# Performance work log

Measured on AMD Instinct MI355X. Metric: run time of the kernel, lower is better.

## Reference

```python
import jax, jax.numpy as jnp
import numpy as np
from jax.scipy.special import logsumexp

K, V, D, R = 512, 50257, 768, 192
S_ITERS = 10
LAMBDA_MAHAL = 0.3
GAMMA_SINKHORN = 0.3


def setup_inputs() -> dict:
    key = jax.random.key(0)
    ks = jax.random.split(key, 6)
    word_embeds = jax.random.normal(ks[0], (V, D), dtype=jnp.float32)
    # warm-start anchors: mean word embed + small noise (as in torch init)
    anchors = jnp.broadcast_to(word_embeds.mean(axis=0, keepdims=True), (K, D)) \
        + jax.random.normal(ks[1], (K, D), dtype=jnp.float32) * 0.05
    return {
        "word_embeds": word_embeds,
        "concept_anchors": anchors,
        "M_U": jax.random.normal(ks[2], (D, R), dtype=jnp.float32) * 0.01,
        "log_eps": jnp.float32(-1.5),
        "log_scale": jnp.float32(0.0),
        "topic_bias": jnp.zeros((K, 1), dtype=jnp.float32),
        "word_proj_w": jnp.eye(D, dtype=jnp.float32),
    }


def _normalize(x, eps=1e-12):
    n = jnp.sqrt(jnp.sum(x * x, axis=-1, keepdims=True))
    return x / jnp.maximum(n, eps)


def _mahalanobis_cost(A, B, M_U):
    # M = I + U U^T  (low-rank update); C[k,v] = (a-b)^T M (a-b)
    M = jnp.eye(A.shape[-1], dtype=A.dtype) + M_U @ M_U.T
    MA = A @ M          # [K, D]
    MB = B @ M          # [V, D]
    AA = jnp.sum(MA * A, axis=-1, keepdims=True)       # [K, 1]
    BB = jnp.sum(MB * B, axis=-1, keepdims=True).T     # [1, V]
    AB = MA @ B.T                                      # [K, V]
    return jax.nn.relu(AA + BB - 2.0 * AB)


def _sinkhorn_log(log_K):
    def body(_, carry):
        log_u, log_v = carry
        log_u = -logsumexp(log_K + log_v, axis=1, keepdims=True)  # [K,1]
        log_v = -logsumexp(log_K + log_u, axis=0, keepdims=True)  # [1,V]
        return log_u, log_v
    log_u0 = jnp.zeros((log_K.shape[0], 1), log_K.dtype)
    log_v0 = jnp.zeros((1, log_K.shape[1]), log_K.dtype)
    log_u, log_v = jax.lax.fori_loop(0, S_ITERS, body, (log_u0, log_v0))
    return log_K + log_u + log_v


def reference(word_embeds, concept_anchors, M_U, log_eps, log_scale,
              topic_bias, word_proj_w):
    w = _normalize(word_embeds @ word_proj_w.T)     # [V, D]
    a = _normalize(concept_anchors)                 # [K, D]
    scale = jnp.minimum(jnp.exp(log_scale), 20.0)
    direct_logits = scale * (a @ w.T) + topic_bias  # [K, V]
    mahal = _mahalanobis_cost(a, w, M_U)            # [K, V]
    eps = jax.nn.softplus(log_eps) + 0.001
    log_P = _sinkhorn_log(-mahal / eps)             # [K, V]
    logits = direct_logits - LAMBDA_MAHAL * mahal + GAMMA_SINKHORN * log_P
    logits = jnp.clip(logits, -30.0, 30.0)
    return jax.nn.softmax(logits, axis=-1)
```

## Files before the change

kernel.cpp:

```cpp
#include <hip/hip_runtime.h>
#include <math.h>

#define KK 512
#define VV 50257
#define VP 50272
#define DD 768
#define RR 192

#define LAM 0.3f
#define GAM 0.3f
#define L2E 1.44269504088896340736f
#define ENC_NEG_INF 0x007FFFFFu

typedef __bf16 bf16x8 __attribute__((ext_vector_type(8)));
typedef _Float16 f16x8 __attribute__((ext_vector_type(8)));
typedef _Float16 f16x2 __attribute__((ext_vector_type(2)));
typedef unsigned short u16x8 __attribute__((ext_vector_type(8)));
typedef float f32x4 __attribute__((ext_vector_type(4)));

static __device__ __forceinline__ float get_eps(const float* p_log_eps) {
  return log1pf(expf(p_log_eps[0])) + 0.001f;
}

static __device__ __forceinline__ float fast_exp2(float x) {
  return __builtin_amdgcn_exp2f(x);
}

static __device__ __forceinline__ unsigned enc_f(float f) {
  unsigned u = __builtin_bit_cast(unsigned, f);
  return (u & 0x80000000u) ? ~u : (u | 0x80000000u);
}
static __device__ __forceinline__ float dec_f(unsigned e) {
  unsigned u = (e & 0x80000000u) ? (e ^ 0x80000000u) : ~e;
  return __builtin_bit_cast(float, u);
}

static __device__ __forceinline__ unsigned short f2bf(float x) {
  unsigned u = __builtin_bit_cast(unsigned, x);
  u += 0x7fffu + ((u >> 16) & 1u);
  return (unsigned short)(u >> 16);
}
static __device__ __forceinline__ float bf2f(unsigned short h) {
  unsigned u = ((unsigned)h) << 16;
  return __builtin_bit_cast(float, u);
}

__global__ __launch_bounds__(256)
void prep(const float* __restrict__ U, float* __restrict__ lv2,
          unsigned* __restrict__ slots, const float* __restrict__ anchors,
          _Float16* __restrict__ Ut16, _Float16* __restrict__ a16) {
  int bid = blockIdx.x;
  int t = threadIdx.x;
  if (bid < 576) {
    int idx = bid * 256 + t;
    int r = idx / DD;
    int d = idx - r * DD;
    Ut16[idx] = (_Float16)U[(size_t)d * RR + r];
  } else if (bid < 773) {
    int i = (bid - 576) * 256 + t;
    if (i < 50264) lv2[i] = 0.f;
  } else if (bid == 773) {
    if (t < 24) slots[t] = (t == 0) ? 0x80000000u : ENC_NEG_INF;
    if (t == 24) slots[24] = 1u;
  } else {
    int r = bid - 774;
    const float* x = anchors + (size_t)r * DD;
    float v0 = x[t], v1 = x[t + 256], v2 = x[t + 512];
    __shared__ float red[256];
    red[t] = v0 * v0 + v1 * v1 + v2 * v2;
    __syncthreads();
    for (int off = 128; off > 0; off >>= 1) {
      if (t < off) red[t] += red[t + off];
      __syncthreads();
    }
    float inv = 1.0f / fmaxf(sqrtf(red[0]), 1e-12f);
    _Float16* y = a16 + (size_t)r * DD;
    y[t] = (_Float16)(v0 * inv);
    y[t + 256] = (_Float16)(v1 * inv);
    y[t + 512] = (_Float16)(v2 * inv);
  }
}

__global__ __launch_bounds__(256)
void check_eye(const float* __restrict__ Wp, unsigned* __restrict__ flag) {
  int i = blockIdx.x * 256 + threadIdx.x;
  if (i >= DD * DD) return;
  int r = i / DD;
  int c = i - r * DD;
  float expect = (r == c) ? 1.f : 0.f;
  if (Wp[i] != expect) atomicAnd(flag, 0u);
}

#define BM 128
#define BN 128
#define BK 32
#define LDKB 40
#define LDK 40

__global__ __launch_bounds__(256, 2)
void gemm_we_fallback(const float* __restrict__ A, const float* __restrict__ B,
                      _Float16* __restrict__ C, int M, int N, int Kd,
                      const unsigned* __restrict__ eyeflag) {
  if (*eyeflag) return;
  __shared__ unsigned short As[2][BM][LDKB];
  __shared__ unsigned short Bs[2][BN][LDKB];
  const int tid = threadIdx.x;
  const int bm = blockIdx.y * BM;
  const int bn = blockIdx.x * BN;
  const int srow = tid >> 1;
  const int skb = (tid & 1) << 4;
  const int wave = tid >> 6;
  const int lane = tid & 63;
  const int wm = (wave >> 1) << 6;
  const int wn = (wave & 1) << 6;
  const int lm = lane & 15;
  const int quad = lane >> 4;
  f32x4 acc[4][4];
#pragma unroll
  for (int i = 0; i < 4; ++i)
#pragma unroll
    for (int j = 0; j < 4; ++j) acc[i][j] = (f32x4){0.f, 0.f, 0.f, 0.f};
  const int ra = bm + srow;
  const int rb = bn + srow;
  for (int k0 = 0; k0 < Kd; k0 += BK) {
    float va[16], vb[16];
    if (ra < M) {
      const float4* p = (const float4*)(A + (size_t)ra * Kd + k0 + skb);
      ((float4*)va)[0] = p[0]; ((float4*)va)[1] = p[1];
      ((float4*)va)[2] = p[2]; ((float4*)va)[3] = p[3];
    } else {
#pragma unroll
      for (int q = 0; q < 16; ++q) va[q] = 0.f;
    }
    if (rb < N) {
      const float4* p = (const float4*)(B + (size_t)rb * Kd + k0 + skb);
      ((float4*)vb)[0] = p[0]; ((float4*)vb)[1] = p[1];
      ((float4*)vb)[2] = p[2]; ((float4*)vb)[3] = p[3];
    } else {
#pragma unroll
      for (int q = 0; q < 16; ++q) vb[q] = 0.f;
    }
    __syncthreads();
    {
      u16x8 h0, h1, l0, l1;
#pragma unroll
      for (int q = 0; q < 8; ++q) {
        unsigned short h = f2bf(va[q]);
        h0[q] = h; l0[q] = f2bf(va[q] - bf2f(h));
        h = f2bf(va[q + 8]);
        h1[q] = h; l1[q] = f2bf(va[q + 8] - bf2f(h));
      }
      *(u16x8*)&As[0][srow][skb] = h0; *(u16x8*)&As[0][srow][skb + 8] = h1;
      *(u16x8*)&As[1][srow][skb] = l0; *(u16x8*)&As[1][srow][skb + 8] = l1;
#pragma unroll
      for (int q = 0; q < 8; ++q) {
        unsigned short h = f2bf(vb[q]);
        h0[q] = h; l0[q] = f2bf(vb[q] - bf2f(h));
        h = f2bf(vb[q + 8]);
        h1[q] = h; l1[q] = f2bf(vb[q + 8] - bf2f(h));
      }
      *(u16x8*)&Bs[0][srow][skb] = h0; *(u16x8*)&Bs[0][srow][skb + 8] = h1;
      *(u16x8*)&Bs[1][srow][skb] = l0; *(u16x8*)&Bs[1][srow][skb + 8] = l1;
    }
    __syncthreads();
    bf16x8 Ah[4], Al[4], Bh[4], Bl[4];
#pragma unroll
    for (int i = 0; i < 4; ++i) {
      Ah[i] = *(const bf16x8*)&As[0][wm + i * 16 + lm][quad * 8];
      Al[i] = *(const bf16x8*)&As[1][wm + i * 16 + lm][quad * 8];
      Bh[i] = *(const bf16x8*)&Bs[0][wn + i * 16 + lm][quad * 8];
      Bl[i] = *(const bf16x8*)&Bs[1][wn + i * 16 + lm][quad * 8];
    }
#pragma unroll
    for (int i = 0; i < 4; ++i)
#pragma unroll
      for (int j = 0; j < 4; ++j) {
        acc[i][j] = __builtin_amdgcn_mfma_f32_16x16x32_bf16(Ah[i], Bh[j], acc[i][j], 0, 0, 0);
        acc[i][j] = __builtin_amdgcn_mfma_f32_16x16x32_bf16(Ah[i], Bl[j], acc[i][j], 0, 0, 0);
        acc[i][j] = __builtin_amdgcn_mfma_f32_16x16x32_bf16(Al[i], Bh[j], acc[i][j], 0, 0, 0);
      }
  }
#pragma unroll
  for (int i = 0; i < 4; ++i)
#pragma unroll
    for (int j = 0; j < 4; ++j) {
      int col = bn + wn + j * 16 + lm;
#pragma unroll
      for (int r = 0; r < 4; ++r) {
        int row = bm + wm + i * 16 + quad * 4 + r;
        if (row < M && col < N) C[(size_t)row * N + col] = (_Float16)acc[i][j][r];
      }
    }
}

__global__ __launch_bounds__(256)
void norm_w(const float* __restrict__ WE, _Float16* __restrict__ w16,
            const unsigned* __restrict__ eyeflag) {
  int r = blockIdx.x;
  int t = threadIdx.x;
  float v0, v1, v2;
  if (*eyeflag) {
    const float* x = WE + (size_t)r * DD;
    v0 = x[t]; v1 = x[t + 256]; v2 = x[t + 512];
  } else {
    const _Float16* x = w16 + (size_t)r * DD;
    v0 = (float)x[t]; v1 = (float)x[t + 256]; v2 = (float)x[t + 512];
  }
  __shared__ float red[256];
  red[t] = v0 * v0 + v1 * v1 + v2 * v2;
  __syncthreads();
  for (int off = 128; off > 0; off >>= 1) {
    if (t < off) red[t] += red[t + off];
    __syncthreads();
  }
  float inv = 1.0f / fmaxf(sqrtf(red[0]), 1e-12f);
  _Float16* y = w16 + (size_t)r * DD;
  y[t] = (_Float16)(v0 * inv);
  y[t + 256] = (_Float16)(v1 * inv);
  y[t + 512] = (_Float16)(v2 * inv);
}

template <int F16OUT>
__global__ __launch_bounds__(256, 2)
void gemm16(const _Float16* __restrict__ A, const _Float16* __restrict__ B,
            void* __restrict__ Cv, int M, int N, int Kd) {
  __shared__ _Float16 As[BM][LDK];
  __shared__ _Float16 Bs[BN][LDK];
  const int tid = threadIdx.x;
  const int bm = blockIdx.y * BM;
  const int bn = blockIdx.x * BN;
  const int srow = tid >> 1;
  const int skb = (tid & 1) << 4;
  const int wave = tid >> 6;
  const int lane = tid & 63;
  const int wm = (wave >> 1) << 6;
  const int wn = (wave & 1) << 6;
  const int lm = lane & 15;
  const int quad = lane >> 4;
  f32x4 acc[4][4];
#pragma unroll
  for (int i = 0; i < 4; ++i)
#pragma unroll
    for (int j = 0; j < 4; ++j) acc[i][j] = (f32x4){0.f, 0.f, 0.f, 0.f};
  const int ra = bm + srow;
  const int rb = bn + srow;
  for (int k0 = 0; k0 < Kd; k0 += BK) {
    f16x8 a0 = (f16x8)(_Float16)0, a1 = a0, b0 = a0, b1 = a0;
    if (ra < M) {
      const f16x8* p = (const f16x8*)(A + (size_t)ra * Kd + k0 + skb);
      a0 = p[0]; a1 = p[1];
    }
    if (rb < N) {
      const f16x8* p = (const f16x8*)(B + (size_t)rb * Kd + k0 + skb);
      b0 = p[0]; b1 = p[1];
    }
    __syncthreads();
    *(f16x8*)&As[srow][skb] = a0; *(f16x8*)&As[srow][skb + 8] = a1;
    *(f16x8*)&Bs[srow][skb] = b0; *(f16x8*)&Bs[srow][skb + 8] = b1;
    __syncthreads();
    f16x8 Af[4], Bf[4];
#pragma unroll
    for (int i = 0; i < 4; ++i) {
      Af[i] = *(const f16x8*)&As[wm + i * 16 + lm][quad * 8];
      Bf[i] = *(const f16x8*)&Bs[wn + i * 16 + lm][quad * 8];
    }
#pragma unroll
    for (int i = 0; i < 4; ++i)
#pragma unroll
      for (int j = 0; j < 4; ++j)
        acc[i][j] = __builtin_amdgcn_mfma_f32_16x16x32_f16(Af[i], Bf[j], acc[i][j], 0, 0, 0);
  }
#pragma unroll
  for (int i = 0; i < 4; ++i)
#pragma unroll
    for (int j = 0; j < 4; ++j) {
      int col = bn + wn + j * 16 + lm;
#pragma unroll
      for (int r = 0; r < 4; ++r) {
        int row = bm + wm + i * 16 + quad * 4 + r;
        if (row < M && col < N) {
          if (F16OUT)
            ((_Float16*)Cv)[(size_t)row * N + col] = (_Float16)acc[i][j][r];
          else
            ((float*)Cv)[(size_t)row * N + col] = acc[i][j][r];
        }
      }
    }
}

__global__ __launch_bounds__(256, 2)
void gemm_sp(const _Float16* __restrict__ Aw, const _Float16* __restrict__ Bw,
             const _Float16* __restrict__ Au, const _Float16* __restrict__ Bu,
             float* __restrict__ Sd, _Float16* __restrict__ mhq,
             const float* __restrict__ AAv, const float* __restrict__ BBv,
             const float* __restrict__ tbias,
             const float* __restrict__ p_log_scale,
             const float* __restrict__ p_log_eps, int M, int N) {
  __shared__ _Float16 As[BM][LDK];
  __shared__ _Float16 Bs[BN][LDK];
  const int tid = threadIdx.x;
  const int bm = blockIdx.y * BM;
  const int bn = blockIdx.x * BN;
  const int srow = tid >> 1;
  const int skb = (tid & 1) << 4;
  const int wave = tid >> 6;
  const int lane = tid & 63;
  const int wm = (wave >> 1) << 6;
  const int wn = (wave & 1) << 6;
  const int lm = lane & 15;
  const int quad = lane >> 4;
  const int ra = bm + srow;
  const int rb = bn + srow;
  f32x4 accP[4][4];
#pragma unroll
  for (int i = 0; i < 4; ++i)
#pragma unroll
    for (int j = 0; j < 4; ++j) accP[i][j] = (f32x4){0.f, 0.f, 0.f, 0.f};
  for (int k0 = 0; k0 < RR; k0 += BK) {
    f16x8 a0 = (f16x8)(_Float16)0, a1 = a0, b0 = a0, b1 = a0;
    if (ra < M) {
      const f16x8* p = (const f16x8*)(Au + (size_t)ra * RR + k0 + skb);
      a0 = p[0]; a1 = p[1];
    }
    if (rb < N) {
      const f16x8* p = (const f16x8*)(Bu + (size_t)rb * RR + k0 + skb);
      b0 = p[0]; b1 = p[1];
    }
    __syncthreads();
    *(f16x8*)&As[srow][skb] = a0; *(f16x8*)&As[srow][skb + 8] = a1;
    *(f16x8*)&Bs[srow][skb] = b0; *(f16x8*)&Bs[srow][skb + 8] = b1;
    __syncthreads();
    f16x8 Af[4], Bf[4];
#pragma unroll
    for (int i = 0; i < 4; ++i) {
      Af[i] = *(const f16x8*)&As[wm + i * 16 + lm][quad * 8];
      Bf[i] = *(const f16x8*)&Bs[wn + i * 16 + lm][quad * 8];
    }
#pragma unroll
    for (int i = 0; i < 4; ++i)
#pragma unroll
      for (int j = 0; j < 4; ++j)
        accP[i][j] = __builtin_amdgcn_mfma_f32_16x16x32_f16(Af[i], Bf[j], accP[i][j], 0, 0, 0);
  }
  f32x4 accS[4][4];
#pragma unroll
  for (int i = 0; i < 4; ++i)
#pragma unroll
    for (int j = 0; j < 4; ++j) accS[i][j] = (f32x4){0.f, 0.f, 0.f, 0.f};
  for (int k0 = 0; k0 < DD; k0 += BK) {
    f16x8 a0 = (f16x8)(_Float16)0, a1 = a0, b0 = a0, b1 = a0;
    if (ra < M) {
      const f16x8* p = (const f16x8*)(Aw + (size_t)ra * DD + k0 + skb);
      a0 = p[0]; a1 = p[1];
    }
    if (rb < N) {
      const f16x8* p = (const f16x8*)(Bw + (size_t)rb * DD + k0 + skb);
      b0 = p[0]; b1 = p[1];
    }
    __syncthreads();
    *(f16x8*)&As[srow][skb] = a0; *(f16x8*)&As[srow][skb + 8] = a1;
    *(f16x8*)&Bs[srow][skb] = b0; *(f16x8*)&Bs[srow][skb + 8] = b1;
    __syncthreads();
    f16x8 Af[4], Bf[4];
#pragma unroll
    for (int i = 0; i < 4; ++i) {
      Af[i] = *(const f16x8*)&As[wm + i * 16 + lm][quad * 8];
      Bf[i] = *(const f16x8*)&Bs[wn + i * 16 + lm][quad * 8];
    }
#pragma unroll
    for (int i = 0; i < 4; ++i)
#pragma unroll
      for (int j = 0; j < 4; ++j)
        accS[i][j] = __builtin_amdgcn_mfma_f32_16x16x32_f16(Af[i], Bf[j], accS[i][j], 0, 0, 0);
  }
  float scale = fminf(expf(p_log_scale[0]), 20.f);
  float qs = L2E / get_eps(p_log_eps);
#pragma unroll
  for (int i = 0; i < 4; ++i)
#pragma unroll
    for (int j = 0; j < 4; ++j) {
      int col = bn + wn + j * 16 + lm;
      if (col >= N) continue;
      float BB = BBv[col];
#pragma unroll
      for (int r = 0; r < 4; ++r) {
        int row = bm + wm + i * 16 + quad * 4 + r;
        float S = accS[i][j][r];
        float mh = fmaxf(AAv[row] + BB - 2.f * (S + accP[i][j][r]), 0.f);
        Sd[(size_t)row * N + col] = fmaf(scale, S, tbias[row]);
        mhq[(size_t)row * VP + col] = (_Float16)(mh * qs);
      }
    }
}

__global__ __launch_bounds__(256, 2)
void gemm16_p(const _Float16* __restrict__ A, const _Float16* __restrict__ B,
              float* __restrict__ Sd, _Float16* __restrict__ mhq,
              const float* __restrict__ AAv, const float* __restrict__ BBv,
              const float* __restrict__ tbias,
              const float* __restrict__ p_log_scale,
              const float* __restrict__ p_log_eps, int M, int N, int Kd) {
  __shared__ _Float16 As[BM][LDK];
  __shared__ _Float16 Bs[BN][LDK];
  const int tid = threadIdx.x;
  const int bm = blockIdx.y * BM;
  const int bn = blockIdx.x * BN;
  const int srow = tid >> 1;
  const int skb = (tid & 1) << 4;
  const int wave = tid >> 6;
  const int lane = tid & 63;
  const int wm = (wave >> 1) << 6;
  const int wn = (wave & 1) << 6;
  const int lm = lane & 15;
  const int quad = lane >> 4;
  f32x4 acc[4][4];
#pragma unroll
  for (int i = 0; i < 4; ++i)
#pragma unroll
    for (int j = 0; j < 4; ++j) acc[i][j] = (f32x4){0.f, 0.f, 0.f, 0.f};
  const int ra = bm + srow;
  const int rb = bn + srow;
  for (int k0 = 0; k0 < Kd; k0 += BK) {
    f16x8 a0 = (f16x8)(_Float16)0, a1 = a0, b0 = a0, b1 = a0;
    if (ra < M) {
      const f16x8* p = (const f16x8*)(A + (size_t)ra * Kd + k0 + skb);
      a0 = p[0]; a1 = p[1];
    }
    if (rb < N) {
      const f16x8* p = (const f16x8*)(B + (size_t)rb * Kd + k0 + skb);
      b0 = p[0]; b1 = p[1];
    }
    __syncthreads();
    *(f16x8*)&As[srow][skb] = a0; *(f16x8*)&As[srow][skb + 8] = a1;
    *(f16x8*)&Bs[srow][skb] = b0; *(f16x8*)&Bs[srow][skb + 8] = b1;
    __syncthreads();
    f16x8 Af[4], Bf[4];
#pragma unroll
    for (int i = 0; i < 4; ++i) {
      Af[i] = *(const f16x8*)&As[wm + i * 16 + lm][quad * 8];
      Bf[i] = *(const f16x8*)&Bs[wn + i * 16 + lm][quad * 8];
    }
#pragma unroll
    for (int i = 0; i < 4; ++i)
#pragma unroll
      for (int j = 0; j < 4; ++j)
        acc[i][j] = __builtin_amdgcn_mfma_f32_16x16x32_f16(Af[i], Bf[j], acc[i][j], 0, 0, 0);
  }
  float scale = fminf(expf(p_log_scale[0]), 20.f);
  float qs = L2E / get_eps(p_log_eps);
#pragma unroll
  for (int i = 0; i < 4; ++i)
#pragma unroll
    for (int j = 0; j < 4; ++j) {
      int col = bn + wn + j * 16 + lm;
      if (col >= N) continue;
      float BB = BBv[col];
#pragma unroll
      for (int r = 0; r < 4; ++r) {
        int row = bm + wm + i * 16 + quad * 4 + r;
        size_t idx = (size_t)row * N + col;
        float S = Sd[idx];
        float mh = fmaxf(AAv[row] + BB - 2.f * (S + acc[i][j][r]), 0.f);
        Sd[idx] = fmaf(scale, S, tbias[row]);
        mhq[(size_t)row * VP + col] = (_Float16)(mh * qs);
      }
    }
}

__global__ __launch_bounds__(256)
void row_sumsq16(const _Float16* __restrict__ X, float* __restrict__ out, int cols) {
  int r = blockIdx.x;
  int t = threadIdx.x;
  float x = (t < cols) ? (float)X[(size_t)r * cols + t] : 0.f;
  __shared__ float red[256];
  red[t] = x * x;
  __syncthreads();
  for (int off = 128; off > 0; off >>= 1) {
    if (t < off) red[t] += red[t + off];
    __syncthreads();
  }
  if (t == 0) out[r] = 1.0f + red[0];
}

__global__ __launch_bounds__(1024)
void sink_row(const _Float16* __restrict__ mhq, const float* __restrict__ lv2,
              float* __restrict__ lu2,
              const unsigned* __restrict__ Mv_slot, unsigned* __restrict__ Mu_slot) {
  int k = blockIdx.x;
  int t = threadIdx.x;
  float Mv2 = dec_f(*Mv_slot);
  const _Float16* row = mhq + (size_t)k * VP;
  float s[8] = {0.f, 0.f, 0.f, 0.f, 0.f, 0.f, 0.f, 0.f};
#pragma unroll
  for (int j = 0; j < 6; ++j) {
    int v = j * 8192 + t * 8;
    f16x8 hv = *(const f16x8*)(row + v);
    float4 l0 = *(const float4*)(lv2 + v);
    float4 l1 = *(const float4*)(lv2 + v + 4);
    float lv[8] = {l0.x, l0.y, l0.z, l0.w, l1.x, l1.y, l1.z, l1.w};
#pragma unroll
    for (int i = 0; i < 8; ++i)
      s[i] += fast_exp2(lv[i] - Mv2 - (float)hv[i]);
  }
  {
    int v = 49152 + t;
    s[0] += fast_exp2(lv2[v] - Mv2 - (float)row[v]);
    v = 50176 + t;
    if (v < VV) s[1] += fast_exp2(lv2[v] - Mv2 - (float)row[v]);
  }
  float sum = ((s[0] + s[1]) + (s[2] + s[3])) + ((s[4] + s[5]) + (s[6] + s[7]));
  __shared__ float red[1024];
  red[t] = sum;
  __syncthreads();
  for (int off = 512; off > 0; off >>= 1) {
    if (t < off) red[t] += red[t + off];
    __syncthreads();
  }
  if (t == 0) {
    float lu = -(Mv2 + log2f(red[0]));
    lu2[k] = lu;
    atomicMax(Mu_slot, enc_f(lu));
  }
}

__global__ __launch_bounds__(256)
void sink_col(const _Float16* __restrict__ mhq, const float* __restrict__ lu2,
              float* __restrict__ lv2,
              const unsigned* __restrict__ Mu_slot, unsigned* __restrict__ Mv_next) {
  __shared__ float lu_s[KK];
  int t = threadIdx.x;
  for (int i = t; i < KK; i += 256) lu_s[i] = lu2[i];
  __syncthreads();
  float Mu2 = dec_f(*Mu_slot);
  int cp = blockIdx.x * 64 + (t & 63);
  int v0 = cp * 2;
  int kc = t >> 6;
  float sA = 0.f, sB = 0.f;
  if (v0 < VV) {
    const _Float16* base = mhq + v0;
#pragma unroll 4
    for (int k = kc * 128; k < kc * 128 + 128; ++k) {
      f16x2 hv = *(const f16x2*)(base + (size_t)k * VP);
      float lu = lu_s[k] - Mu2;
      sA += fast_exp2(lu - (float)hv[0]);
      sB += fast_exp2(lu - (float)hv[1]);
    }
  }
  __shared__ float pA[256], pB[256];
  __shared__ unsigned em[64];
  pA[t] = sA; pB[t] = sB;
  __syncthreads();
  if (t < 64) {
    unsigned e = ENC_NEG_INF;
    if (v0 < VV) {
      float a = (pA[t] + pA[t + 64]) + (pA[t + 128] + pA[t + 192]);
      float lv = -(Mu2 + log2f(a));
      lv2[v0] = lv;
      e = enc_f(lv);
      if (v0 + 1 < VV) {
        float b = (pB[t] + pB[t + 64]) + (pB[t + 128] + pB[t + 192]);
        float lv1 = -(Mu2 + log2f(b));
        lv2[v0 + 1] = lv1;
        unsigned e1 = enc_f(lv1);
        if (e1 > e) e = e1;
      }
    }
    em[t] = e;
  }
  __syncthreads();
  for (int off = 32; off > 0; off >>= 1) {
    if (t < off && em[t + off] > em[t]) em[t] = em[t + off];
    __syncthreads();
  }
  if (t == 0) atomicMax(Mv_next, em[0]);
}

__global__ __launch_bounds__(1024)
void final_sum(const float* __restrict__ direct, const _Float16* __restrict__ mhq,
               const float* __restrict__ lu2, const float* __restrict__ lv2,
               float* __restrict__ row_s, const float* __restrict__ p_log_eps) {
  int k = blockIdx.x;
  int t = threadIdx.x;
  float eps = get_eps(p_log_eps);
  float c2 = (LAM * eps + GAM) / L2E;
  float c3 = GAM / L2E;
  float base_lu = c3 * lu2[k];
  const float* drow = direct + (size_t)k * VV;
  const _Float16* mrow = mhq + (size_t)k * VP;
  float s[8] = {0.f, 0.f, 0.f, 0.f, 0.f, 0.f, 0.f, 0.f};
#pragma unroll
  for (int j = 0; j < 6; ++j) {
    int v = j * 8192 + t * 8;
    f16x8 hv = *(const f16x8*)(mrow + v);
    float4 d0 = *(const float4*)(drow + v);
    float4 d1 = *(const float4*)(drow + v + 4);
    float4 l0 = *(const float4*)(lv2 + v);
    float4 l1 = *(const float4*)(lv2 + v + 4);
    float dd[8] = {d0.x, d0.y, d0.z, d0.w, d1.x, d1.y, d1.z, d1.w};
    float lv[8] = {l0.x, l0.y, l0.z, l0.w, l1.x, l1.y, l1.z, l1.w};
#pragma unroll
    for (int i = 0; i < 8; ++i) {
      float x = fmaf(-c2, (float)hv[i], fmaf(c3, lv[i], dd[i] + base_lu));
      x = fminf(30.f, fmaxf(-30.f, x));
      s[i] += fast_exp2(fmaf(x, L2E, -30.f * L2E));
    }
  }
  {
    int v = 49152 + t;
    float x = fmaf(-c2, (float)mrow[v], fmaf(c3, lv2[v], drow[v] + base_lu));
    x = fminf(30.f, fmaxf(-30.f, x));
    s[0] += fast_exp2(fmaf(x, L2E, -30.f * L2E));
    v = 50176 + t;
    if (v < VV) {
      x = fmaf(-c2, (float)mrow[v], fmaf(c3, lv2[v], drow[v] + base_lu));
      x = fminf(30.f, fmaxf(-30.f, x));
      s[1] += fast_exp2(fmaf(x, L2E, -30.f * L2E));
    }
  }
  float sum = ((s[0] + s[1]) + (s[2] + s[3])) + ((s[4] + s[5]) + (s[6] + s[7]));
  __shared__ float red[1024];
  red[t] = sum;
  __syncthreads();
  for (int off = 512; off > 0; off >>= 1) {
    if (t < off) red[t] += red[t + off];
    __syncthreads();
  }
  if (t == 0) row_s[k] = red[0];
}

__global__ __launch_bounds__(256)
void final_write(float* __restrict__ out, const _Float16* __restrict__ mhq,
                 const float* __restrict__ lu2, const float* __restrict__ lv2,
                 const float* __restrict__ row_s, const float* __restrict__ p_log_eps) {
  int v = blockIdx.x * 256 + threadIdx.x;
  int k = blockIdx.y;
  if (v >= VV) return;
  float eps = get_eps(p_log_eps);
  float c2 = (LAM * eps + GAM) / L2E;
  float c3 = GAM / L2E;
  size_t idx = (size_t)k * VV + v;
  float x = fmaf(-c2, (float)mhq[(size_t)k * VP + v],
                 fmaf(c3, lv2[v], out[idx] + c3 * lu2[k]));
  x = fminf(30.f, fmaxf(-30.f, x));
  out[idx] = fast_exp2(fmaf(x, L2E, -30.f * L2E)) / row_s[k];
}

extern "C" void kernel_launch(void* const* d_in, const int* in_sizes, int n_in,
                              void* d_out, int out_size, void* d_ws, size_t ws_size,
                              hipStream_t stream) {
  (void)in_sizes; (void)n_in; (void)out_size;
  const float* WE        = (const float*)d_in[0];
  const float* anchors   = (const float*)d_in[1];
  const float* MU        = (const float*)d_in[2];
  const float* log_eps   = (const float*)d_in[3];
  const float* log_scale = (const float*)d_in[4];
  const float* tbias     = (const float*)d_in[5];
  const float* Wp        = (const float*)d_in[6];
  float* out = (float*)d_out;

  const size_t H_W16 = (size_t)VV * DD;
  const size_t H_MHQ = (size_t)KK * VP;
  const size_t H_WU  = (size_t)VV * RR;
  const size_t H_A16 = (size_t)KK * DD;
  const size_t H_AU  = (size_t)KK * RR;
  const size_t H_UT  = (size_t)RR * DD;
  const size_t FB_FLOATS = 102064 + 32;
  const size_t need_roomy =
      2 * (H_W16 + H_MHQ + H_WU + H_A16 + H_AU + H_UT) + 4 * FB_FLOATS;
  const bool roomy = ws_size >= need_roomy;

  _Float16* hb = (_Float16*)d_ws;
  _Float16* w16 = hb;
  size_t ho = H_W16;
  _Float16* mhq;
  if (roomy) { mhq = hb + ho; ho += H_MHQ; }
  else       { mhq = hb; }
  _Float16* wU16 = hb + ho; ho += H_WU;
  _Float16* a16  = hb + ho; ho += H_A16;
  _Float16* aU16 = hb + ho; ho += H_AU;
  _Float16* Ut16 = hb + ho; ho += H_UT;
  float* fb = (float*)(hb + ho);
  float* BBv   = fb;
  float* AAv   = fb + 50264;
  float* lu2   = fb + 50776;
  float* lv2   = fb + 51288;
  float* row_s = fb + 101552;
  unsigned* slots = (unsigned*)(fb + 102064);
  unsigned* Mv_slots = slots;
  unsigned* Mu_slots = slots + 12;
  unsigned* eye_flag = slots + 24;

  const int VB = (VV + 255) / 256;
  const int MB_V = (VV + BM - 1) / BM;

  prep<<<1286, 256, 0, stream>>>(MU, lv2, slots, anchors, Ut16, a16);
  check_eye<<<(DD * DD + 255) / 256, 256, 0, stream>>>(Wp, eye_flag);
  gemm_we_fallback<<<dim3(DD / BN, MB_V), 256, 0, stream>>>(WE, Wp, w16, VV, DD, DD, eye_flag);
  norm_w<<<VV, 256, 0, stream>>>(WE, w16, eye_flag);
  gemm16<1><<<dim3(2, MB_V), 256, 0, stream>>>(w16, Ut16, wU16, VV, RR, DD);
  gemm16<1><<<dim3(2, 4), 256, 0, stream>>>(a16, Ut16, aU16, KK, RR, DD);
  row_sumsq16<<<VV, 256, 0, stream>>>(wU16, BBv, RR);
  row_sumsq16<<<KK, 256, 0, stream>>>(aU16, AAv, RR);
  if (roomy) {
    gemm_sp<<<dim3(MB_V, 4), 256, 0, stream>>>(a16, w16, aU16, wU16, out, mhq,
                                               AAv, BBv, tbias, log_scale,
                                               log_eps, KK, VV);
  } else {
    gemm16<0><<<dim3(MB_V, 4), 256, 0, stream>>>(a16, w16, out, KK, VV, DD);
    gemm16_p<<<dim3(MB_V, 4), 256, 0, stream>>>(aU16, wU16, out, mhq, AAv, BBv,
                                                tbias, log_scale, log_eps, KK, VV, RR);
  }
  for (int it = 0; it < 10; ++it) {
    sink_row<<<KK, 1024, 0, stream>>>(mhq, lv2, lu2, Mv_slots + it, Mu_slots + it);
    sink_col<<<MB_V, 256, 0, stream>>>(mhq, lu2, lv2, Mu_slots + it, Mv_slots + it + 1);
  }
  final_sum<<<KK, 1024, 0, stream>>>(out, mhq, lu2, lv2, row_s, log_eps);
  final_write<<<dim3(VB, KK), 256, 0, stream>>>(out, mhq, lu2, lv2, row_s, log_eps);
}
```

Baseline: 929.3 us.

## Use direct global-to-LDS loads with XOR swizzle in fused score GEMM

The fused similarity/Mahalanobis GEMM now stages its A and B tiles with global_load_lds instead of loading into registers and then storing to shared memory. The LDS tile is unpadded and uses an XOR swizzle to avoid bank conflicts, and the grid is transposed so the four row-blocks sharing a vocab tile are launched next to each other for better L2 reuse of the word embeddings. Bounds checks on rows are dropped, which relies on the input buffers being padded past N and adds an extra barrier per k-step.

```diff
diff --git a/kernel.cpp b/kernel.cpp
--- a/kernel.cpp
+++ b/kernel.cpp
@@ -43,6 +43,12 @@
 static __device__ __forceinline__ float bf2f(unsigned short h) {
   unsigned u = ((unsigned)h) << 16;
   return __builtin_bit_cast(float, u);
+}
+
+static __device__ __forceinline__ void gload_lds16(const void* g, void* l) {
+  __builtin_amdgcn_global_load_lds(
+      (const __attribute__((address_space(1))) unsigned int*)g,
+      (__attribute__((address_space(3))) unsigned int*)l, 16, 0, 0);
 }
 
 __global__ __launch_bounds__(256)
@@ -296,83 +302,96 @@
              const float* __restrict__ tbias,
              const float* __restrict__ p_log_scale,
              const float* __restrict__ p_log_eps, int M, int N) {
-  __shared__ _Float16 As[BM][LDK];
-  __shared__ _Float16 Bs[BN][LDK];
+  __shared__ _Float16 As[BM][32];
+  __shared__ _Float16 Bs[BN][32];
   const int tid = threadIdx.x;
-  const int bm = blockIdx.y * BM;
-  const int bn = blockIdx.x * BN;
-  const int srow = tid >> 1;
-  const int skb = (tid & 1) << 4;
+  const int bm = blockIdx.x * BM;
+  const int bn = blockIdx.y * BN;
   const int wave = tid >> 6;
   const int lane = tid & 63;
   const int wm = (wave >> 1) << 6;
   const int wn = (wave & 1) << 6;
   const int lm = lane & 15;
   const int quad = lane >> 4;
-  const int ra = bm + srow;
-  const int rb = bn + srow;
+
+  const int c0 = wave * 2;
+  const int r0 = c0 * 16 + (lane >> 2);
+  const int r1 = r0 + 16;
+  const int gp = lane & 3;
+  const int gg0 = gp ^ ((r0 >> 1) & 3);
+  const int gg1 = gp ^ ((r1 >> 1) & 3);
+  _Float16* ldsA0 = &As[0][0] + c0 * 512;
+  _Float16* ldsA1 = ldsA0 + 512;
+  _Float16* ldsB0 = &Bs[0][0] + c0 * 512;
+  _Float16* ldsB1 = ldsB0 + 512;
+
   f32x4 accP[4][4];
 #pragma unroll
   for (int i = 0; i < 4; ++i)
 #pragma unroll
     for (int j = 0; j < 4; ++j) accP[i][j] = (f32x4){0.f, 0.f, 0.f, 0.f};
-  for (int k0 = 0; k0 < RR; k0 += BK) {
-    f16x8 a0 = (f16x8)(_Float16)0, a1 = a0, b0 = a0, b1 = a0;
-    if (ra < M) {
-      const f16x8* p = (const f16x8*)(Au + (size_t)ra * RR + k0 + skb);
-      a0 = p[0]; a1 = p[1];
-    }
-    if (rb < N) {
-      const f16x8* p = (const f16x8*)(Bu + (size_t)rb * RR + k0 + skb);
-      b0 = p[0]; b1 = p[1];
-    }
-    __syncthreads();
-    *(f16x8*)&As[srow][skb] = a0; *(f16x8*)&As[srow][skb + 8] = a1;
-    *(f16x8*)&Bs[srow][skb] = b0; *(f16x8*)&Bs[srow][skb + 8] = b1;
-    __syncthreads();
-    f16x8 Af[4], Bf[4];
-#pragma unroll
-    for (int i = 0; i < 4; ++i) {
-      Af[i] = *(const f16x8*)&As[wm + i * 16 + lm][quad * 8];
-      Bf[i] = *(const f16x8*)&Bs[wn + i * 16 + lm][quad * 8];
-    }
-#pragma unroll
-    for (int i = 0; i < 4; ++i)
-#pragma unroll
-      for (int j = 0; j < 4; ++j)
-        accP[i][j] = __builtin_amdgcn_mfma_f32_16x16x32_f16(Af[i], Bf[j], accP[i][j], 0, 0, 0);
-  }
+
+  {
+    const _Float16* pa0 = Au + (size_t)(bm + r0) * RR + gg0 * 8;
+    const _Float16* pa1 = Au + (size_t)(bm + r1) * RR + gg1 * 8;
+    const _Float16* pb0 = Bu + (size_t)(bn + r0) * RR + gg0 * 8;
+    const _Float16* pb1 = Bu + (size_t)(bn + r1) * RR + gg1 * 8;
+    for (int k0 = 0; k0 < RR; k0 += BK) {
+      gload_lds16(pa0 + k0, ldsA0);
+      gload_lds16(pa1 + k0, ldsA1);
+      gload_lds16(pb0 + k0, ldsB0);
+      gload_lds16(pb1 + k0, ldsB1);
+      __syncthreads();
+      f16x8 Af[4], Bf[4];
+#pragma unroll
+      for (int i = 0; i < 4; ++i) {
+        int ra_ = wm + i * 16 + lm;
+        int rb_ = wn + i * 16 + lm;
+        Af[i] = *(const f16x8*)&As[ra_][(quad ^ ((ra_ >> 1) & 3)) * 8];
+        Bf[i] = *(const f16x8*)&Bs[rb_][(quad ^ ((rb_ >> 1) & 3)) * 8];
+      }
+#pragma unroll
+      for (int i = 0; i < 4; ++i)
+#pragma unroll
+        for (int j = 0; j < 4; ++j)
+          accP[i][j] = __builtin_amdgcn_mfma_f32_16x16x32_f16(Af[i], Bf[j], accP[i][j], 0, 0, 0);
+      __syncthreads();
+    }
+  }
+
   f32x4 accS[4][4];
 #pragma unroll
   for (int i = 0; i < 4; ++i)
 #pragma unroll
     for (int j = 0; j < 4; ++j) accS[i][j] = (f32x4){0.f, 0.f, 0.f, 0.f};
-  for (int k0 = 0; k0 < DD; k0 += BK) {
-    f16x8 a0 = (f16x8)(_Float16)0, a1 = a0, b0 = a0, b1 = a0;
-    if (ra < M) {
-      const f16x8* p = (const f16x8*)(Aw + (size_t)ra * DD + k0 + skb);
-      a0 = p[0]; a1 = p[1];
-    }
-    if (rb < N) {
-      const f16x8* p = (const f16x8*)(Bw + (size_t)rb * DD + k0 + skb);
-      b0 = p[0]; b1 = p[1];
-    }
-    __syncthreads();
-    *(f16x8*)&As[srow][skb] = a0; *(f16x8*)&As[srow][skb + 8] = a1;
-    *(f16x8*)&Bs[srow][skb] = b0; *(f16x8*)&Bs[srow][skb + 8] = b1;
-    __syncthreads();
-    f16x8 Af[4], Bf[4];
-#pragma unroll
-    for (int i = 0; i < 4; ++i) {
-      Af[i] = *(const f16x8*)&As[wm + i * 16 + lm][quad * 8];
-      Bf[i] = *(const f16x8*)&Bs[wn + i * 16 + lm][quad * 8];
-    }
-#pragma unroll
-    for (int i = 0; i < 4; ++i)
-#pragma unroll
-      for (int j = 0; j < 4; ++j)
-        accS[i][j] = __builtin_amdgcn_mfma_f32_16x16x32_f16(Af[i], Bf[j], accS[i][j], 0, 0, 0);
-  }
+  {
+    const _Float16* pa0 = Aw + (size_t)(bm + r0) * DD + gg0 * 8;
+    const _Float16* pa1 = Aw + (size_t)(bm + r1) * DD + gg1 * 8;
+    const _Float16* pb0 = Bw + (size_t)(bn + r0) * DD + gg0 * 8;
+    const _Float16* pb1 = Bw + (size_t)(bn + r1) * DD + gg1 * 8;
+    for (int k0 = 0; k0 < DD; k0 += BK) {
+      gload_lds16(pa0 + k0, ldsA0);
+      gload_lds16(pa1 + k0, ldsA1);
+      gload_lds16(pb0 + k0, ldsB0);
+      gload_lds16(pb1 + k0, ldsB1);
+      __syncthreads();
+      f16x8 Af[4], Bf[4];
+#pragma unroll
+      for (int i = 0; i < 4; ++i) {
+        int ra_ = wm + i * 16 + lm;
+        int rb_ = wn + i * 16 + lm;
+        Af[i] = *(const f16x8*)&As[ra_][(quad ^ ((ra_ >> 1) & 3)) * 8];
+        Bf[i] = *(const f16x8*)&Bs[rb_][(quad ^ ((rb_ >> 1) & 3)) * 8];
+      }
+#pragma unroll
+      for (int i = 0; i < 4; ++i)
+#pragma unroll
+        for (int j = 0; j < 4; ++j)
+          accS[i][j] = __builtin_amdgcn_mfma_f32_16x16x32_f16(Af[i], Bf[j], accS[i][j], 0, 0, 0);
+      __syncthreads();
+    }
+  }
+
   float scale = fminf(expf(p_log_scale[0]), 20.f);
   float qs = L2E / get_eps(p_log_eps);
 #pragma unroll
@@ -702,7 +721,7 @@
   row_sumsq16<<<VV, 256, 0, stream>>>(wU16, BBv, RR);
   row_sumsq16<<<KK, 256, 0, stream>>>(aU16, AAv, RR);
   if (roomy) {
-    gemm_sp<<<dim3(MB_V, 4), 256, 0, stream>>>(a16, w16, aU16, wU16, out, mhq,
+    gemm_sp<<<dim3(4, MB_V), 256, 0, stream>>>(a16, w16, aU16, wU16, out, mhq,
                                                AAv, BBv, tbias, log_scale,
                                                log_eps, KK, VV);
   } else {
```

New measurement: 907.6 us. 1.02x faster.
